# Kernel tuning notes

Hardware: AMD Instinct MI355X
Metric: run time of the kernel (lower is better)

The kernel has to match this reference:

```python
import jax, jax.numpy as jnp
import numpy as np

B, S, C = 1, 2048, 2048
H, D = 16, 128
FF = 8192
EPS = 1e-6


def _rms(x, w):
    return x * jax.lax.rsqrt(jnp.mean(x * x, axis=-1, keepdims=True) + EPS) * w


def _rope(x, cos, sin):
    # x: [B,S,H,D]; cos/sin: [S,D]
    x1, x2 = jnp.split(x, 2, axis=-1)
    rot = jnp.concatenate([-x2, x1], axis=-1)
    return x * cos[None, :, None, :] + rot * sin[None, :, None, :]


def setup_inputs() -> dict:
    key = jax.random.key(0)
    ks = jax.random.split(key, 12)
    # RoPE tables
    inv_freq = 1.0 / (10000.0 ** (jnp.arange(0, D, 2, dtype=jnp.float32) / D))
    freqs = jnp.arange(S, dtype=jnp.float32)[:, None] * inv_freq[None, :]
    emb = jnp.concatenate([freqs, freqs], axis=-1)  # [S,D]
    # causal additive mask
    causal = jnp.tril(jnp.ones((S, S), dtype=bool))
    mask = jnp.where(causal, 0.0, -1e9).astype(jnp.float32)[None, None]
    w = lambda k, shp: (jax.random.normal(k, shp, dtype=jnp.float32) * 0.02)
    return {
        "hidden_states": jax.random.normal(ks[0], (B, S, C), dtype=jnp.float32),
        "cos": jnp.cos(emb),
        "sin": jnp.sin(emb),
        "attention_mask": mask,
        "ln1_w": jnp.ones((C,), dtype=jnp.float32),
        "wq": w(ks[1], (C, C)),
        "wk": w(ks[2], (C, C)),
        "wv": w(ks[3], (C, C)),
        "wo": w(ks[4], (C, C)),
        "ln2_w": jnp.ones((C,), dtype=jnp.float32),
        "w_gate": w(ks[5], (FF, C)),
        "w_up": w(ks[6], (FF, C)),
        "w_down": w(ks[7], (C, FF)),
    }


def reference(hidden_states, cos, sin, attention_mask, ln1_w, wq, wk, wv, wo,
              ln2_w, w_gate, w_up, w_down):
    # --- input RMSNorm ---
    x = _rms(hidden_states, ln1_w)
    # --- W2 (Gaussian-kernel) attention ---
    q = (x @ wq.T).reshape(B, S, H, D)
    k = (x @ wk.T).reshape(B, S, H, D)
    v = (x @ wv.T).reshape(B, S, H, D)
    q = _rope(q, cos, sin).transpose(0, 2, 1, 3)  # [B,H,S,D]
    k = _rope(k, cos, sin).transpose(0, 2, 1, 3)
    v = v.transpose(0, 2, 1, 3)
    qk = jnp.einsum('bhid,bhjd->bhij', q, k)
    q2 = jnp.sum(q * q, axis=-1)  # [B,H,S]
    k2 = jnp.sum(k * k, axis=-1)
    dist2 = q2[..., :, None] - 2.0 * qk + k2[..., None, :]  # ||q-k||^2
    scores = -dist2 / (2.0 * np.sqrt(D).astype(np.float32)) + attention_mask
    attn = jax.nn.softmax(scores, axis=-1)
    ctx = jnp.einsum('bhij,bhjd->bhid', attn, v)
    attn_out = ctx.transpose(0, 2, 1, 3).reshape(B, S, C) @ wo.T
    h = hidden_states + attn_out
    # --- post-attn RMSNorm + SwiGLU FFN ---
    y = _rms(h, ln2_w)
    ffn = (jax.nn.silu(y @ w_gate.T) * (y @ w_up.T)) @ w_down.T
    return h + ffn
```

## Files before the change

### kernel.cpp

```cpp
#include <hip/hip_runtime.h>
#include <cstdint>
#include <cstddef>

typedef __bf16 bf16x8 __attribute__((ext_vector_type(8)));
typedef float f32x4 __attribute__((ext_vector_type(4)));

union V16 { uint4 u; bf16x8 b; unsigned short s[8]; };

__device__ __forceinline__ float b2f(unsigned short u) {
  unsigned int x = ((unsigned int)u) << 16;
  float f;
  __builtin_memcpy(&f, &x, 4);
  return f;
}
__device__ __forceinline__ unsigned short f2b(float f) {
  unsigned int u;
  __builtin_memcpy(&u, &f, 4);
  u = u + 0x7FFFu + ((u >> 16) & 1u);
  return (unsigned short)(u >> 16);
}

__device__ __forceinline__ f32x4 mfma16(bf16x8 a, bf16x8 b, f32x4 c) {
  return __builtin_amdgcn_mfma_f32_16x16x32_bf16(a, b, c, 0, 0, 0);
}

__device__ __forceinline__ void gld_lds16(const unsigned short* g, unsigned short* l) {
  __builtin_amdgcn_global_load_lds((__attribute__((address_space(1))) void*)g,
                                   (__attribute__((address_space(3))) void*)l,
                                   16, 0, 0);
}

__global__ __launch_bounds__(256) void cvt_k(const float* __restrict__ in,
                                             unsigned short* __restrict__ out, int n) {
  const int i = (blockIdx.x * 256 + threadIdx.x) * 4;
  if (i + 3 < n) {
    const float4 v = *(const float4*)(in + i);
    ushort4 o;
    o.x = f2b(v.x); o.y = f2b(v.y); o.z = f2b(v.z); o.w = f2b(v.w);
    *(ushort4*)(out + i) = o;
  }
}

__global__ __launch_bounds__(256) void rms_k(const float* __restrict__ xin,
                                             const float* __restrict__ wgt,
                                             unsigned short* __restrict__ out) {
  const int s = blockIdx.x;
  const int t = threadIdx.x;
  float vals[8];
  float ss = 0.f;
#pragma unroll
  for (int i = 0; i < 8; ++i) {
    const int c = t + i * 256;
    const float f = xin[(size_t)s * 2048 + c];
    vals[i] = f;
    ss += f * f;
  }
#pragma unroll
  for (int off = 32; off > 0; off >>= 1) ss += __shfl_xor(ss, off);
  __shared__ float red[4];
  if ((t & 63) == 0) red[t >> 6] = ss;
  __syncthreads();
  ss = red[0] + red[1] + red[2] + red[3];
  const float sc = rsqrtf(ss * (1.f / 2048.f) + 1e-6f);
#pragma unroll
  for (int i = 0; i < 8; ++i) {
    const int c = t + i * 256;
    out[(size_t)s * 2048 + c] = f2b(vals[i] * sc * wgt[c]);
  }
}

__global__ __launch_bounds__(256) void rope_qk(unsigned short* qb, unsigned short* kb,
                                               const float* __restrict__ cosb,
                                               const float* __restrict__ sinb) {
  const int idx = blockIdx.x * 256 + threadIdx.x;
  const int d = idx & 63;
  const int h = (idx >> 6) & 15;
  const int s = idx >> 10;
  const size_t base = (size_t)s * 2048 + h * 128;
  const int cb = s * 128;
  const float c1 = cosb[cb + d],      s1 = sinb[cb + d];
  const float c2 = cosb[cb + d + 64], s2 = sinb[cb + d + 64];
  {
    const float x1 = b2f(qb[base + d]), x2 = b2f(qb[base + d + 64]);
    qb[base + d]      = f2b(x1 * c1 - x2 * s1);
    qb[base + d + 64] = f2b(x2 * c2 + x1 * s2);
  }
  {
    const float x1 = b2f(kb[base + d]), x2 = b2f(kb[base + d + 64]);
    kb[base + d]      = f2b(x1 * c1 - x2 * s1);
    kb[base + d + 64] = f2b(x2 * c2 + x1 * s2);
  }
}

template <int EPI, int RT>
__global__ __launch_bounds__(256, 2) void gemm_nt(
    const unsigned short* __restrict__ A,
    const unsigned short* __restrict__ B0,
    const unsigned short* __restrict__ B1,
    const unsigned short* __restrict__ B2,
    unsigned short* C0, unsigned short* C1, unsigned short* C2,
    const unsigned short* auxb, const float* auxf, float* Cf,
    int N, int K) {
  constexpr int TM = RT * 32;
  constexpr int APASS = TM / 64;
  const unsigned short* B = (blockIdx.z == 0) ? B0 : (blockIdx.z == 1 ? B1 : B2);
  unsigned short* C = (blockIdx.z == 0) ? C0 : (blockIdx.z == 1 ? C1 : C2);

  const int m0 = blockIdx.y * TM;
  const int n0 = blockIdx.x * 128;
  const int t = threadIdx.x;
  const int lane = t & 63;
  const int w = t >> 6;
  const int quad = lane >> 4;
  const int l15 = lane & 15;
  const int wr = w >> 1;
  const int wc = w & 1;

  __shared__ __align__(16) unsigned short As[TM * 32];
  __shared__ __align__(16) unsigned short Bs[128 * 32];

  const f32x4 vzero = {0.f, 0.f, 0.f, 0.f};
  f32x4 acc[RT][4];
#pragma unroll
  for (int i = 0; i < RT; ++i)
#pragma unroll
    for (int j = 0; j < 4; ++j) acc[i][j] = vzero;

  const int srow = w * 16 + (lane >> 2);
  const int scol = (lane & 3) * 8;
  const unsigned short* Ag = A + (size_t)(m0 + srow) * K + scol;
  const unsigned short* Bg = B + (size_t)(n0 + srow) * K + scol;

  for (int k0 = 0; k0 < K; k0 += 32) {
#pragma unroll
    for (int p = 0; p < APASS; ++p)
      gld_lds16(Ag + (size_t)p * 64 * K + k0, As + p * 2048 + w * 512);
#pragma unroll
    for (int p = 0; p < 2; ++p)
      gld_lds16(Bg + (size_t)p * 64 * K + k0, Bs + p * 2048 + w * 512);
    __syncthreads();

    bf16x8 af[RT], bfr[4];
#pragma unroll
    for (int rt = 0; rt < RT; ++rt)
      af[rt] = *(const bf16x8*)&As[(wr * (RT * 16) + rt * 16 + l15) * 32 + quad * 8];
#pragma unroll
    for (int ct = 0; ct < 4; ++ct)
      bfr[ct] = *(const bf16x8*)&Bs[(wc * 64 + ct * 16 + l15) * 32 + quad * 8];
#pragma unroll
    for (int rt = 0; rt < RT; ++rt)
#pragma unroll
      for (int ct = 0; ct < 4; ++ct)
        acc[rt][ct] = mfma16(af[rt], bfr[ct], acc[rt][ct]);
    __syncthreads();
  }

#pragma unroll
  for (int rt = 0; rt < RT; ++rt) {
#pragma unroll
    for (int ct = 0; ct < 4; ++ct) {
#pragma unroll
      for (int r = 0; r < 4; ++r) {
        const int m = m0 + wr * (RT * 16) + rt * 16 + quad * 4 + r;
        const int n = n0 + wc * 64 + ct * 16 + l15;
        const size_t idx = (size_t)m * N + n;
        const float a = acc[rt][ct][r];
        if constexpr (EPI == 0) {
          C[idx] = f2b(a);
        } else if constexpr (EPI == 1) {
          Cf[idx] = auxf[idx] + a;
        } else {
          const float g = b2f(auxb[idx]);
          const float sg = g / (1.f + __expf(-g));
          C[idx] = f2b(sg * a);
        }
      }
    }
  }
}

__global__ __launch_bounds__(256, 2) void flash_w2(
    const unsigned short* __restrict__ q,
    const unsigned short* __restrict__ kk,
    const unsigned short* __restrict__ v,
    unsigned short* __restrict__ ctx) {
  constexpr int Cw = 2048;
  constexpr float inv2sd = 0.04419417382415922f;
  const int h = blockIdx.y;
  const int i0 = blockIdx.x * 64;
  const int t = threadIdx.x;
  const int lane = t & 63;
  const int w = t >> 6;
  const int quad = lane >> 4;
  const int l15 = lane & 15;

  __shared__ __align__(16) unsigned short Ks[64 * 136];
  __shared__ __align__(16) unsigned short VTs[128 * 72];
  __shared__ __align__(16) unsigned short Ps[4][16 * 72];

  bf16x8 aq[4];
  float q2p = 0.f;
  {
    const unsigned short* qp = q + (size_t)(i0 + w * 16 + l15) * Cw + h * 128;
#pragma unroll
    for (int kt = 0; kt < 4; ++kt) {
      V16 u;
      u.u = *(const uint4*)(qp + kt * 32 + quad * 8);
      aq[kt] = u.b;
#pragma unroll
      for (int j = 0; j < 8; ++j) { const float f = (float)u.b[j]; q2p += f * f; }
    }
  }
  q2p += __shfl_xor(q2p, 16);
  q2p += __shfl_xor(q2p, 32);
  float q2r[4];
#pragma unroll
  for (int r = 0; r < 4; ++r) q2r[r] = __shfl(q2p, quad * 4 + r);

  const f32x4 vzero = {0.f, 0.f, 0.f, 0.f};
  f32x4 o[8];
#pragma unroll
  for (int nt = 0; nt < 8; ++nt) o[nt] = vzero;
  float mrow[4] = {-1e30f, -1e30f, -1e30f, -1e30f};
  float lrow[4] = {0.f, 0.f, 0.f, 0.f};

  const int njt = blockIdx.x + 1;
  for (int jt = 0; jt < njt; ++jt) {
    const int j0 = jt * 64;
    __syncthreads();
    {
      const int jr = t >> 2;
      const int c0 = (t & 3) * 32;
      const unsigned short* kp = kk + (size_t)(j0 + jr) * Cw + h * 128 + c0;
      const unsigned short* vp = v + (size_t)(j0 + jr) * Cw + h * 128 + c0;
#pragma unroll
      for (int i = 0; i < 4; ++i) {
        *(uint4*)&Ks[jr * 136 + c0 + i * 8] = *(const uint4*)(kp + i * 8);
        V16 vu;
        vu.u = *(const uint4*)(vp + i * 8);
#pragma unroll
        for (int e = 0; e < 8; ++e) VTs[(c0 + i * 8 + e) * 72 + jr] = vu.s[e];
      }
    }
    __syncthreads();

    f32x4 sc[4];
    float k2[4];
#pragma unroll
    for (int ct = 0; ct < 4; ++ct) {
      f32x4 a = vzero;
      float k2p = 0.f;
#pragma unroll
      for (int kt = 0; kt < 4; ++kt) {
        V16 u;
        u.u = *(const uint4*)&Ks[(ct * 16 + l15) * 136 + kt * 32 + quad * 8];
        a = mfma16(aq[kt], u.b, a);
#pragma unroll
        for (int j = 0; j < 8; ++j) { const float f = (float)u.b[j]; k2p += f * f; }
      }
      k2p += __shfl_xor(k2p, 16);
      k2p += __shfl_xor(k2p, 32);
      sc[ct] = a;
      k2[ct] = k2p;
    }

#pragma unroll
    for (int ct = 0; ct < 4; ++ct) {
#pragma unroll
      for (int r = 0; r < 4; ++r) {
        const int gi = i0 + w * 16 + quad * 4 + r;
        const int gj = j0 + ct * 16 + l15;
        const float s = -(q2r[r] - 2.f * sc[ct][r] + k2[ct]) * inv2sd;
        sc[ct][r] = (gj <= gi) ? s : -1e30f;
      }
    }

    float al[4];
#pragma unroll
    for (int r = 0; r < 4; ++r) {
      float rm = fmaxf(fmaxf(sc[0][r], sc[1][r]), fmaxf(sc[2][r], sc[3][r]));
      rm = fmaxf(rm, __shfl_xor(rm, 1));
      rm = fmaxf(rm, __shfl_xor(rm, 2));
      rm = fmaxf(rm, __shfl_xor(rm, 4));
      rm = fmaxf(rm, __shfl_xor(rm, 8));
      const float mn = fmaxf(mrow[r], rm);
      al[r] = __expf(mrow[r] - mn);
      mrow[r] = mn;
      float ps = 0.f;
#pragma unroll
      for (int ct = 0; ct < 4; ++ct) {
        const float p = __expf(sc[ct][r] - mn);
        sc[ct][r] = p;
        ps += p;
      }
      ps += __shfl_xor(ps, 1);
      ps += __shfl_xor(ps, 2);
      ps += __shfl_xor(ps, 4);
      ps += __shfl_xor(ps, 8);
      lrow[r] = lrow[r] * al[r] + ps;
    }
#pragma unroll
    for (int nt = 0; nt < 8; ++nt)
#pragma unroll
      for (int r = 0; r < 4; ++r) o[nt][r] *= al[r];

#pragma unroll
    for (int ct = 0; ct < 4; ++ct)
#pragma unroll
      for (int r = 0; r < 4; ++r)
        Ps[w][(quad * 4 + r) * 72 + ct * 16 + l15] = f2b(sc[ct][r]);
    __syncthreads();

#pragma unroll
    for (int kt2 = 0; kt2 < 2; ++kt2) {
      V16 pa;
      pa.u = *(const uint4*)&Ps[w][l15 * 72 + kt2 * 32 + quad * 8];
#pragma unroll
      for (int nt = 0; nt < 8; ++nt) {
        V16 vb;
        vb.u = *(const uint4*)&VTs[(nt * 16 + l15) * 72 + kt2 * 32 + quad * 8];
        o[nt] = mfma16(pa.b, vb.b, o[nt]);
      }
    }
  }

  float invl[4];
#pragma unroll
  for (int r = 0; r < 4; ++r) invl[r] = 1.f / lrow[r];
#pragma unroll
  for (int nt = 0; nt < 8; ++nt) {
#pragma unroll
    for (int r = 0; r < 4; ++r) {
      const int gi = i0 + w * 16 + quad * 4 + r;
      ctx[(size_t)gi * Cw + h * 128 + nt * 16 + l15] = f2b(o[nt][r] * invl[r]);
    }
  }
}

extern "C" void kernel_launch(void* const* d_in, const int* in_sizes, int n_in,
                              void* d_out, int out_size, void* d_ws, size_t ws_size,
                              hipStream_t stream) {
  (void)in_sizes; (void)n_in; (void)out_size; (void)ws_size;
  const float* hid  = (const float*)d_in[0];
  const float* cosb = (const float*)d_in[1];
  const float* sinb = (const float*)d_in[2];
  const float* ln1w = (const float*)d_in[4];
  const float* wq   = (const float*)d_in[5];
  const float* wk   = (const float*)d_in[6];
  const float* wv   = (const float*)d_in[7];
  const float* wo   = (const float*)d_in[8];
  const float* ln2w = (const float*)d_in[9];
  const float* wg   = (const float*)d_in[10];
  const float* wu   = (const float*)d_in[11];
  const float* wd   = (const float*)d_in[12];
  float* outp = (float*)d_out;

  const size_t SC = (size_t)2048 * 2048;
  const size_t FC = (size_t)8192 * 2048;
  unsigned short* p = (unsigned short*)d_ws;
  unsigned short* wqb = p;  p += SC;
  unsigned short* wkb = p;  p += SC;
  unsigned short* wvb = p;  p += SC;
  unsigned short* wob = p;  p += SC;
  unsigned short* wgb = p;  p += FC;
  unsigned short* wub = p;  p += FC;
  unsigned short* wdb = p;  p += FC;
  unsigned short* xn  = p;  p += SC;
  unsigned short* qb  = p;  p += SC;
  unsigned short* kb  = p;  p += SC;
  unsigned short* vb  = p;  p += SC;
  unsigned short* ctxb = p; p += SC;
  float* hf = (float*)p;
  unsigned short* yn = xn;
  unsigned short* gb = qb;

  cvt_k<<<(int)(SC / 1024), 256, 0, stream>>>(wq, wqb, (int)SC);
  cvt_k<<<(int)(SC / 1024), 256, 0, stream>>>(wk, wkb, (int)SC);
  cvt_k<<<(int)(SC / 1024), 256, 0, stream>>>(wv, wvb, (int)SC);
  cvt_k<<<(int)(SC / 1024), 256, 0, stream>>>(wo, wob, (int)SC);
  cvt_k<<<(int)(FC / 1024), 256, 0, stream>>>(wg, wgb, (int)FC);
  cvt_k<<<(int)(FC / 1024), 256, 0, stream>>>(wu, wub, (int)FC);
  cvt_k<<<(int)(FC / 1024), 256, 0, stream>>>(wd, wdb, (int)FC);

  rms_k<<<2048, 256, 0, stream>>>(hid, ln1w, xn);
  gemm_nt<0, 4><<<dim3(16, 16, 3), 256, 0, stream>>>(xn, wqb, wkb, wvb, qb, kb, vb,
                                                     nullptr, nullptr, nullptr, 2048, 2048);
  rope_qk<<<8192, 256, 0, stream>>>(qb, kb, cosb, sinb);
  flash_w2<<<dim3(32, 16), 256, 0, stream>>>(qb, kb, vb, ctxb);
  gemm_nt<1, 2><<<dim3(16, 32, 1), 256, 0, stream>>>(ctxb, wob, wob, wob,
                                                     nullptr, nullptr, nullptr,
                                                     nullptr, hid, hf, 2048, 2048);
  rms_k<<<2048, 256, 0, stream>>>(hf, ln2w, yn);
  gemm_nt<0, 4><<<dim3(64, 16, 1), 256, 0, stream>>>(yn, wgb, wgb, wgb, gb, gb, gb,
                                                     nullptr, nullptr, nullptr, 8192, 2048);
  gemm_nt<2, 4><<<dim3(64, 16, 1), 256, 0, stream>>>(yn, wub, wub, wub, gb, gb, gb,
                                                     gb, nullptr, nullptr, 8192, 2048);
  gemm_nt<1, 2><<<dim3(16, 32, 1), 256, 0, stream>>>(gb, wdb, wdb, wdb,
                                                     nullptr, nullptr, nullptr,
                                                     nullptr, hf, outp, 2048, 8192);
}
```

Baseline: 886.4 us.

## Precompute key norms in RoPE, drop q-norm term, swizzle V transpose in attention

The RoPE kernel now computes each key's squared norm, scaled, in fp32 and stores it. The attention kernel reads that value instead of recomputing it per tile, and drops the per-row q² term because it cancels in softmax. The causal mask now applies only on the diagonal tile, the transposed V tile in shared memory uses an XOR swizzle to cut bank conflicts, and heads 8-15 walk query blocks in reverse to balance load. It also removes one per-tile barrier, raises launch bounds to 3 blocks, and adds a small workspace buffer. Key norms now come from fp32 values rather than the rounded bf16 keys, which slightly changes numerics.

```diff
diff --git a/kernel.cpp b/kernel.cpp
--- a/kernel.cpp
+++ b/kernel.cpp
@@ -71,7 +71,8 @@
 
 __global__ __launch_bounds__(256) void rope_qk(unsigned short* qb, unsigned short* kb,
                                                const float* __restrict__ cosb,
-                                               const float* __restrict__ sinb) {
+                                               const float* __restrict__ sinb,
+                                               float* __restrict__ k2c) {
   const int idx = blockIdx.x * 256 + threadIdx.x;
   const int d = idx & 63;
   const int h = (idx >> 6) & 15;
@@ -87,8 +88,14 @@
   }
   {
     const float x1 = b2f(kb[base + d]), x2 = b2f(kb[base + d + 64]);
-    kb[base + d]      = f2b(x1 * c1 - x2 * s1);
-    kb[base + d + 64] = f2b(x2 * c2 + x1 * s2);
+    const float k1 = x1 * c1 - x2 * s1;
+    const float k2 = x2 * c2 + x1 * s2;
+    kb[base + d]      = f2b(k1);
+    kb[base + d + 64] = f2b(k2);
+    float ss = k1 * k1 + k2 * k2;
+#pragma unroll
+    for (int off = 32; off > 0; off >>= 1) ss += __shfl_xor(ss, off);
+    if (d == 0) k2c[h * 2048 + s] = ss * 0.04419417382415922f;
   }
 }
 
@@ -179,15 +186,17 @@
   }
 }
 
-__global__ __launch_bounds__(256, 2) void flash_w2(
+__global__ __launch_bounds__(256, 3) void flash_w2(
     const unsigned short* __restrict__ q,
     const unsigned short* __restrict__ kk,
     const unsigned short* __restrict__ v,
+    const float* __restrict__ k2c,
     unsigned short* __restrict__ ctx) {
   constexpr int Cw = 2048;
-  constexpr float inv2sd = 0.04419417382415922f;
+  constexpr float TWOC = 0.08838834764831843f;
   const int h = blockIdx.y;
-  const int i0 = blockIdx.x * 64;
+  const int i = (h >= 8) ? (31 - blockIdx.x) : blockIdx.x;
+  const int i0 = i * 64;
   const int t = threadIdx.x;
   const int lane = t & 63;
   const int w = t >> 6;
@@ -199,7 +208,6 @@
   __shared__ __align__(16) unsigned short Ps[4][16 * 72];
 
   bf16x8 aq[4];
-  float q2p = 0.f;
   {
     const unsigned short* qp = q + (size_t)(i0 + w * 16 + l15) * Cw + h * 128;
 #pragma unroll
@@ -207,15 +215,8 @@
       V16 u;
       u.u = *(const uint4*)(qp + kt * 32 + quad * 8);
       aq[kt] = u.b;
-#pragma unroll
-      for (int j = 0; j < 8; ++j) { const float f = (float)u.b[j]; q2p += f * f; }
-    }
-  }
-  q2p += __shfl_xor(q2p, 16);
-  q2p += __shfl_xor(q2p, 32);
-  float q2r[4];
-#pragma unroll
-  for (int r = 0; r < 4; ++r) q2r[r] = __shfl(q2p, quad * 4 + r);
+    }
+  }
 
   const f32x4 vzero = {0.f, 0.f, 0.f, 0.f};
   f32x4 o[8];
@@ -224,54 +225,61 @@
   float mrow[4] = {-1e30f, -1e30f, -1e30f, -1e30f};
   float lrow[4] = {0.f, 0.f, 0.f, 0.f};
 
-  const int njt = blockIdx.x + 1;
+  const int njt = i + 1;
+  const int jr = t >> 2;
+  const int c0 = (t & 3) * 32;
+  const int jlo = jr & 7;
+  const int jhi = jr >> 3;
   for (int jt = 0; jt < njt; ++jt) {
     const int j0 = jt * 64;
     __syncthreads();
     {
-      const int jr = t >> 2;
-      const int c0 = (t & 3) * 32;
       const unsigned short* kp = kk + (size_t)(j0 + jr) * Cw + h * 128 + c0;
       const unsigned short* vp = v + (size_t)(j0 + jr) * Cw + h * 128 + c0;
 #pragma unroll
-      for (int i = 0; i < 4; ++i) {
-        *(uint4*)&Ks[jr * 136 + c0 + i * 8] = *(const uint4*)(kp + i * 8);
+      for (int ii = 0; ii < 4; ++ii) {
+        *(uint4*)&Ks[jr * 136 + c0 + ii * 8] = *(const uint4*)(kp + ii * 8);
         V16 vu;
-        vu.u = *(const uint4*)(vp + i * 8);
-#pragma unroll
-        for (int e = 0; e < 8; ++e) VTs[(c0 + i * 8 + e) * 72 + jr] = vu.s[e];
+        vu.u = *(const uint4*)(vp + ii * 8);
+#pragma unroll
+        for (int e = 0; e < 8; ++e) {
+          const int dd = c0 + ii * 8 + e;
+          const int gs = (jhi ^ (dd >> 4)) & 7;
+          VTs[dd * 72 + (jlo | (gs << 3))] = vu.s[e];
+        }
       }
     }
     __syncthreads();
 
+    float k2v[4];
+#pragma unroll
+    for (int ct = 0; ct < 4; ++ct) k2v[ct] = k2c[h * 2048 + j0 + ct * 16 + l15];
+
     f32x4 sc[4];
-    float k2[4];
 #pragma unroll
     for (int ct = 0; ct < 4; ++ct) {
       f32x4 a = vzero;
-      float k2p = 0.f;
 #pragma unroll
       for (int kt = 0; kt < 4; ++kt) {
         V16 u;
         u.u = *(const uint4*)&Ks[(ct * 16 + l15) * 136 + kt * 32 + quad * 8];
         a = mfma16(aq[kt], u.b, a);
-#pragma unroll
-        for (int j = 0; j < 8; ++j) { const float f = (float)u.b[j]; k2p += f * f; }
-      }
-      k2p += __shfl_xor(k2p, 16);
-      k2p += __shfl_xor(k2p, 32);
+      }
       sc[ct] = a;
-      k2[ct] = k2p;
-    }
-
+    }
+
+    const bool diag = (jt == njt - 1);
 #pragma unroll
     for (int ct = 0; ct < 4; ++ct) {
 #pragma unroll
       for (int r = 0; r < 4; ++r) {
-        const int gi = i0 + w * 16 + quad * 4 + r;
-        const int gj = j0 + ct * 16 + l15;
-        const float s = -(q2r[r] - 2.f * sc[ct][r] + k2[ct]) * inv2sd;
-        sc[ct][r] = (gj <= gi) ? s : -1e30f;
+        float s = fmaf(TWOC, sc[ct][r], -k2v[ct]);
+        if (diag) {
+          const int gi = w * 16 + quad * 4 + r;
+          const int gj = ct * 16 + l15;
+          s = (gj <= gi) ? s : -1e30f;
+        }
+        sc[ct][r] = s;
       }
     }
 
@@ -309,7 +317,6 @@
 #pragma unroll
       for (int r = 0; r < 4; ++r)
         Ps[w][(quad * 4 + r) * 72 + ct * 16 + l15] = f2b(sc[ct][r]);
-    __syncthreads();
 
 #pragma unroll
     for (int kt2 = 0; kt2 < 2; ++kt2) {
@@ -318,7 +325,9 @@
 #pragma unroll
       for (int nt = 0; nt < 8; ++nt) {
         V16 vb;
-        vb.u = *(const uint4*)&VTs[(nt * 16 + l15) * 72 + kt2 * 32 + quad * 8];
+        const int dd = nt * 16 + l15;
+        const int gs = (kt2 * 4 + quad) ^ nt;
+        vb.u = *(const uint4*)&VTs[dd * 72 + gs * 8];
         o[nt] = mfma16(pa.b, vb.b, o[nt]);
       }
     }
@@ -370,7 +379,8 @@
   unsigned short* kb  = p;  p += SC;
   unsigned short* vb  = p;  p += SC;
   unsigned short* ctxb = p; p += SC;
-  float* hf = (float*)p;
+  float* hf = (float*)p;   p += 2 * SC;
+  float* k2cb = (float*)p;
   unsigned short* yn = xn;
   unsigned short* gb = qb;
 
@@ -385,8 +395,8 @@
   rms_k<<<2048, 256, 0, stream>>>(hid, ln1w, xn);
   gemm_nt<0, 4><<<dim3(16, 16, 3), 256, 0, stream>>>(xn, wqb, wkb, wvb, qb, kb, vb,
                                                      nullptr, nullptr, nullptr, 2048, 2048);
-  rope_qk<<<8192, 256, 0, stream>>>(qb, kb, cosb, sinb);
-  flash_w2<<<dim3(32, 16), 256, 0, stream>>>(qb, kb, vb, ctxb);
+  rope_qk<<<8192, 256, 0, stream>>>(qb, kb, cosb, sinb, k2cb);
+  flash_w2<<<dim3(32, 16), 256, 0, stream>>>(qb, kb, vb, k2cb, ctxb);
   gemm_nt<1, 2><<<dim3(16, 32, 1), 256, 0, stream>>>(ctxb, wob, wob, wob,
                                                      nullptr, nullptr, nullptr,
                                                      nullptr, hid, hf, 2048, 2048);
```

After: 844.5 us. -4.7%, faster.
